# Kernel optimization log

Hardware: AMD Instinct MI355X
Metric: run time of the kernel (lower is better)

Reference implementation:

```python
import jax, jax.numpy as jnp
import numpy as np
import math

D = 32   # in_planes / d_model
T = 9    # num_contexts
L = 24   # token_len
H = 8    # nhead
HD = D // H
NEUMANN = 3
ALPHA = 0.9

def _lin(x, w, b):
    return x @ w.T + b

def _gelu(x):
    return jax.nn.gelu(x, approximate=False)

def reference(x, ln_g, ln_b, rp_w1, rp_b1, rp_w2, rp_b2, W_causal,
              mask_w, mask_b, val_w1, val_b1, val_w2, val_b2, fuse_gate,
              q_w, q_b, k_w, k_b, v_w, v_b, m_w, m_b,
              W_logit, W_ctx, rel_pos_bias, pre_prompt, conv_w, conv_b, p_w, p_b):
    b = x.shape[0]
    x_btlc = jnp.transpose(x, (0, 2, 3, 1))              # (b,t,l,c)
    # ---- rule pooling (LayerNorm -> Linear -> GELU -> Linear) ----
    pooled = x_btlc.mean(axis=(1, 2))                    # (b,c)
    mu = pooled.mean(-1, keepdims=True)
    var = pooled.var(-1, keepdims=True)
    pn = (pooled - mu) / jnp.sqrt(var + 1e-5) * ln_g + ln_b
    pooled_rule = _lin(_gelu(_lin(pn, rp_w1, rp_b1)), rp_w2, rp_b2)
    # ---- causal graph discovery ----
    A = jax.nn.softplus(W_causal) * (1.0 - jnp.eye(D, dtype=x.dtype))
    # ---- intervention engine ----
    x_obs = x_btlc.mean(axis=(1, 2))                     # (b,c)
    scale = jnp.clip(jnp.std(x_btlc, axis=(1, 2), ddof=1), 1e-3)  # torch unbiased std
    M = jax.nn.sigmoid(_lin(pooled_rule, mask_w, mask_b))
    v_raw = _lin(_gelu(_lin(pooled_rule, val_w1, val_b1)), val_w2, val_b2)
    v32 = jnp.tanh(v_raw) * scale + x_obs
    x_do = (1.0 - M) * x_obs + M * v32
    A32 = ALPHA * A / (A.sum(-1, keepdims=True) + 1e-6)  # row-normalize
    y = x_do
    for _ in range(NEUMANN):                             # fp32 Neumann series
        y = x_do + y @ A32.T
    delta = (y - x_obs)[:, None, None, :]
    fused = x_btlc + jax.nn.sigmoid(fuse_gate) * delta   # (b,t,l,c)
    # ---- cosine-sim multi-head attention with rel-pos bias & head mixing ----
    def heads(w, bb):
        h = _lin(fused, w, bb).reshape(b, T, L, H, HD).transpose(0, 1, 3, 2, 4)
        return h / jnp.linalg.norm(h, axis=-1, keepdims=True).clip(1e-12)
    q = heads(q_w, q_b); k = heads(k_w, k_b); v = heads(v_w, v_b)
    logits = jnp.einsum('bthid,bthjd->bthij', q, k) / math.sqrt(HD)
    idx = jnp.arange(L)
    rel = jnp.clip(idx[:, None] - idx[None, :] + (L - 1), 0, 2 * L - 2)
    logits = logits + rel_pos_bias[:, rel][None, None]   # (h,L,L) broadcast
    logits = jnp.einsum('bthij,hH->btHij', logits, W_logit)
    atten = jax.nn.softmax(logits, axis=-1)
    atten = jnp.einsum('bthij,hH->btHij', atten, W_ctx)
    x_att = jnp.einsum('bthij,bthjd->bthid', atten, v)
    x_att = _lin(x_att.transpose(0, 1, 3, 2, 4).reshape(b, T, L, D), m_w, m_b)
    x_att = jnp.transpose(x_att, (0, 3, 1, 2))           # (b,c,t,l)
    # ---- prediction branch (conv over contexts + linear over tokens) ----
    pre = jnp.broadcast_to(pre_prompt, (b, D, 1, L))
    con = jnp.concatenate([x_att[:, :, :T - 1], pre], axis=2)   # (b,c,T,L)
    p = jax.lax.conv_general_dilated(con, conv_w, (1, 1), 'VALID',
        dimension_numbers=('NCHW', 'OIHW', 'NCHW')) + conv_b[None, :, None, None]
    p = jax.nn.relu(p)                                   # ConvNormAct act; norm=identity at init
    p = _lin(p, p_w, p_b)                                # Linear(token_len, token_len)
    p = x_att[:, :, T - 1:] - p
    return jnp.concatenate([x_att[:, :, :T - 1], p], axis=2)


def setup_inputs() -> dict:
    key = jax.random.key(0)
    ks = jax.random.split(key, 24)
    B = 4096
    def r(i, sh, s=0.02):
        return jax.random.normal(ks[i], sh, jnp.float32) * s
    return dict(
        x=jax.random.normal(ks[0], (B, D, T, L), jnp.float32),
        ln_g=jnp.ones((D,), jnp.float32), ln_b=jnp.zeros((D,), jnp.float32),
        rp_w1=r(1, (D, D)), rp_b1=jnp.zeros((D,), jnp.float32),
        rp_w2=r(2, (D, D)), rp_b2=jnp.zeros((D,), jnp.float32),
        W_causal=r(3, (D, D)),
        mask_w=r(4, (D, D)), mask_b=jnp.zeros((D,), jnp.float32),
        val_w1=r(5, (D, D)), val_b1=jnp.zeros((D,), jnp.float32),
        val_w2=r(6, (D, D)), val_b2=jnp.zeros((D,), jnp.float32),
        fuse_gate=jnp.float32(0.5),
        q_w=r(7, (D, D)), q_b=jnp.zeros((D,), jnp.float32),
        k_w=r(8, (D, D)), k_b=jnp.zeros((D,), jnp.float32),
        v_w=r(9, (D, D)), v_b=jnp.zeros((D,), jnp.float32),
        m_w=r(10, (D, D)), m_b=jnp.zeros((D,), jnp.float32),
        W_logit=jnp.eye(H, dtype=jnp.float32) + r(11, (H, H), 0.01),
        W_ctx=jnp.eye(H, dtype=jnp.float32) + r(12, (H, H), 0.01),
        rel_pos_bias=r(13, (H, 2 * L - 1)),
        pre_prompt=r(14, (1, D, 1, L)),
        conv_w=r(15, (D, D, T, 1)), conv_b=jnp.zeros((D,), jnp.float32),
        p_w=r(16, (L, L)), p_b=jnp.zeros((L,), jnp.float32),
    )
```

## Files before the change

kernel.cpp:

```cpp
#include <hip/hip_runtime.h>
#include <hip/hip_bf16.h>

#define DD 32
#define TT 9
#define LL 24
#define HH 8
#define NPOS 216
#define RPB_W 47
#define ALPHA 0.9f

__device__ __forceinline__ float gelu_exact(float x) {
    return 0.5f * x * (1.0f + erff(x * 0.7071067811865476f));
}
__device__ __forceinline__ float sigmoidf_(float x) { return 1.0f / (1.0f + expf(-x)); }


__global__ void k0_prep(const float* __restrict__ wcausal,
                        const float* __restrict__ w_logit,
                        const float* __restrict__ rpb,
                        float* __restrict__ ws) {
    __shared__ float A[DD][DD];
    __shared__ float rs[DD];
    int tid = threadIdx.x;
    int i = tid >> 5, j = tid & 31;
    float a = (i == j) ? 0.0f : log1pf(expf(wcausal[tid]));
    A[i][j] = a;
    __syncthreads();
    if (j == 0) {
        float s = 0.0f;
        for (int k = 0; k < DD; k++) s += A[i][k];
        rs[i] = ALPHA / (s + 1e-6f);
    }
    __syncthreads();
    ws[tid] = A[i][j] * rs[i];
    if (tid < 64) ws[1024 + tid] = 0.5f * w_logit[tid];
    if (tid < 384) {
        int H = tid / 48, r = tid % 48;
        float v = 0.0f;
        if (r < RPB_W) {
            for (int h = 0; h < HH; h++) v += w_logit[h * HH + H] * rpb[h * RPB_W + r];
        }
        ws[1088 + tid] = v;
    }
}

__global__ __launch_bounds__(256) void k1a(const float* __restrict__ x,
                                           float* __restrict__ sp, float* __restrict__ sq) {
    int b = blockIdx.x, tid = threadIdx.x;
    int c = tid >> 3, r = tid & 7;
    const float4* x4 = (const float4*)(x + (size_t)b * (DD * NPOS) + (size_t)c * NPOS);
    float s = 0.0f, q = 0.0f;
    for (int k = r; k < 54; k += 8) {
        float4 v = x4[k];
        s += v.x + v.y + v.z + v.w;
        q += v.x * v.x + v.y * v.y + v.z * v.z + v.w * v.w;
    }
    for (int m = 1; m < 8; m <<= 1) { s += __shfl_xor(s, m); q += __shfl_xor(q, m); }
    if (r == 0) { sp[b * DD + c] = s; sq[b * DD + c] = q; }
}

__global__ __launch_bounds__(64) void k1b(
    const float* __restrict__ ln_g, const float* __restrict__ ln_b,
    const float* __restrict__ rp_w1, const float* __restrict__ rp_b1,
    const float* __restrict__ rp_w2, const float* __restrict__ rp_b2,
    const float* __restrict__ mask_w, const float* __restrict__ mask_b,
    const float* __restrict__ val_w1, const float* __restrict__ val_b1,
    const float* __restrict__ val_w2, const float* __restrict__ val_b2,
    const float* __restrict__ fuse_gate, const float* __restrict__ ws,
    float* __restrict__ sp , const float* __restrict__ sq)
{
    __shared__ float W[6][1024];
    __shared__ float V[7][32];
    int tid = threadIdx.x;
    for (int idx = tid; idx < 1024; idx += 64) {
        W[0][idx] = rp_w1[idx]; W[1][idx] = rp_w2[idx]; W[2][idx] = mask_w[idx];
        W[3][idx] = val_w1[idx]; W[4][idx] = val_w2[idx]; W[5][idx] = ws[idx];
    }
    if (tid < 32) {
        V[0][tid] = ln_g[tid]; V[1][tid] = ln_b[tid]; V[2][tid] = rp_b1[tid];
        V[3][tid] = rp_b2[tid]; V[4][tid] = mask_b[tid]; V[5][tid] = val_b1[tid];
        V[6][tid] = val_b2[tid];
    }
    __syncthreads();
    int b = blockIdx.x * 64 + tid;

    float pooled[32], scl[32];
    const float4* sp4 = (const float4*)(sp + (size_t)b * 32);
    const float4* sq4 = (const float4*)(sq + (size_t)b * 32);
    #pragma unroll
    for (int k = 0; k < 8; k++) {
        float4 sv = sp4[k], qv = sq4[k];
        float ss[4] = {sv.x, sv.y, sv.z, sv.w};
        float qq[4] = {qv.x, qv.y, qv.z, qv.w};
        #pragma unroll
        for (int m = 0; m < 4; m++) {
            int c = 4 * k + m;
            float p = ss[m] * (1.0f / NPOS);
            pooled[c] = p;
            float var1 = (qq[m] - (float)NPOS * p * p) * (1.0f / (NPOS - 1));
            scl[c] = fmaxf(sqrtf(fmaxf(var1, 0.0f)), 1e-3f);
        }
    }
    float mu = 0.0f;
    #pragma unroll
    for (int c = 0; c < 32; c++) mu += pooled[c];
    mu *= (1.0f / 32.0f);
    float vv = 0.0f;
    #pragma unroll
    for (int c = 0; c < 32; c++) { float d = pooled[c] - mu; vv += d * d; }
    vv *= (1.0f / 32.0f);
    float inv = rsqrtf(vv + 1e-5f);
    float pn[32];
    #pragma unroll
    for (int c = 0; c < 32; c++) pn[c] = (pooled[c] - mu) * inv * V[0][c] + V[1][c];

    float h1[32];
    #pragma unroll
    for (int i = 0; i < 32; i++) {
        float acc = V[2][i];
        #pragma unroll
        for (int j = 0; j < 32; j++) acc += pn[j] * W[0][i * 32 + j];
        h1[i] = gelu_exact(acc);
    }
    float pr[32];
    #pragma unroll
    for (int i = 0; i < 32; i++) {
        float acc = V[3][i];
        #pragma unroll
        for (int j = 0; j < 32; j++) acc += h1[j] * W[1][i * 32 + j];
        pr[i] = acc;
    }
    float g1[32];
    #pragma unroll
    for (int i = 0; i < 32; i++) {
        float acc = V[5][i];
        #pragma unroll
        for (int j = 0; j < 32; j++) acc += pr[j] * W[3][i * 32 + j];
        g1[i] = gelu_exact(acc);
    }
    float xd[32];
    #pragma unroll
    for (int i = 0; i < 32; i++) {
        float am = V[4][i];
        #pragma unroll
        for (int j = 0; j < 32; j++) am += pr[j] * W[2][i * 32 + j];
        float M = sigmoidf_(am);
        float av = V[6][i];
        #pragma unroll
        for (int j = 0; j < 32; j++) av += g1[j] * W[4][i * 32 + j];
        float v32 = tanhf(av) * scl[i] + pooled[i];
        xd[i] = (1.0f - M) * pooled[i] + M * v32;
    }
    float y[32];
    #pragma unroll
    for (int c = 0; c < 32; c++) y[c] = xd[c];
    for (int it = 0; it < 3; it++) {
        float ny[32];
        #pragma unroll
        for (int i = 0; i < 32; i++) {
            float acc = xd[i];
            #pragma unroll
            for (int j = 0; j < 32; j++) acc += y[j] * W[5][i * 32 + j];
            ny[i] = acc;
        }
        #pragma unroll
        for (int c = 0; c < 32; c++) y[c] = ny[c];
    }
    float g = sigmoidf_(fuse_gate[0]);
    float4* dout4 = (float4*)(sp + (size_t)b * 32);
    #pragma unroll
    for (int k = 0; k < 8; k++) {
        float4 o;
        o.x = g * (y[4 * k + 0] - pooled[4 * k + 0]);
        o.y = g * (y[4 * k + 1] - pooled[4 * k + 1]);
        o.z = g * (y[4 * k + 2] - pooled[4 * k + 2]);
        o.w = g * (y[4 * k + 3] - pooled[4 * k + 3]);
        dout4[k] = o;
    }
}

__global__ __launch_bounds__(192) void k2_attn(
    const float* __restrict__ x,
    const float* __restrict__ ws,
    const float* __restrict__ delta,
    const float* __restrict__ q_w, const float* __restrict__ q_b,
    const float* __restrict__ k_w, const float* __restrict__ k_b,
    const float* __restrict__ v_w, const float* __restrict__ v_b,
    const float* __restrict__ m_w, const float* __restrict__ m_b,
    const float* __restrict__ w_ctx,
    float* __restrict__ out)
{
    __shared__ float r1[3456];
    __shared__ float r2[5824];
    __shared__ float msc[640];
    float* fusedf = r1;
    float* qsf = r1 + 864;
    float* ksf = r1 + 1728;
    float* vsf = r1 + 2592;
    float* wqf = r2;
    float* wkf = r2 + 1024;
    float* wvf = r2 + 2048;
    float* lg2 = r2;
    float* wmf = r2 + 4800;
    float* bqf = msc, *bkf = msc + 32, *bvf = msc + 64, *bmf = msc + 96;
    float* wl05f = msc + 128;
    float* wcf = msc + 192;
    float* rpmf = msc + 256;

    int blk = blockIdx.x;
    int b = blk / TT, t = blk % TT;
    int tid = threadIdx.x;

    for (int idx = tid; idx < 768; idx += 192) {
        int m = idx >> 8, r = idx & 255;
        int i = r >> 3, jq = r & 7;
        const float* src = (m == 0) ? q_w : (m == 1) ? k_w : v_w;
        float* dst = (m == 0) ? wqf : (m == 1) ? wkf : wvf;
        float4 v = ((const float4*)src)[r];
        int col = i ^ (4 * jq);
        dst[(4 * jq + 0) * 32 + col] = v.x;
        dst[(4 * jq + 1) * 32 + col] = v.y;
        dst[(4 * jq + 2) * 32 + col] = v.z;
        dst[(4 * jq + 3) * 32 + col] = v.w;
    }
    if (tid < 32) { bqf[tid] = q_b[tid]; bkf[tid] = k_b[tid]; bvf[tid] = v_b[tid]; bmf[tid] = m_b[tid]; }
    else if (tid < 96) wl05f[tid - 32] = ws[1024 + tid - 32];
    else if (tid < 160) wcf[tid - 96] = w_ctx[tid - 96];
    for (int idx = tid; idx < 384; idx += 192) rpmf[idx] = ws[1088 + idx];
    {
        int c = tid / 6, k = tid % 6;
        const float4* p = (const float4*)(x + (size_t)b * (DD * NPOS) + (size_t)c * NPOS + t * LL);
        float4 v = p[k];
        float gd = delta[b * DD + c];
        int l0 = 4 * k;
        fusedf[(l0 + 0) * 36 + c] = v.x + gd;
        fusedf[(l0 + 1) * 36 + c] = v.y + gd;
        fusedf[(l0 + 2) * 36 + c] = v.z + gd;
        fusedf[(l0 + 3) * 36 + c] = v.w + gd;
    }
    __syncthreads();

    {
        int l = tid >> 3, q = tid & 7;
        float4 aq = *(const float4*)&bqf[4 * q];
        float4 ak = *(const float4*)&bkf[4 * q];
        float4 av = *(const float4*)&bvf[4 * q];
        #pragma unroll
        for (int jq = 0; jq < 8; jq++) {
            float4 f4 = *(const float4*)&fusedf[l * 36 + 4 * jq];
            float fv[4] = {f4.x, f4.y, f4.z, f4.w};
            #pragma unroll
            for (int jj = 0; jj < 4; jj++) {
                int j = 4 * jq + jj;
                int sw = (4 * q) ^ (j & 28);
                float f = fv[jj];
                float4 w0 = *(const float4*)&wqf[j * 32 + sw];
                float4 w1 = *(const float4*)&wkf[j * 32 + sw];
                float4 w2 = *(const float4*)&wvf[j * 32 + sw];
                aq.x += f * w0.x; aq.y += f * w0.y; aq.z += f * w0.z; aq.w += f * w0.w;
                ak.x += f * w1.x; ak.y += f * w1.y; ak.z += f * w1.z; ak.w += f * w1.w;
                av.x += f * w2.x; av.y += f * w2.y; av.z += f * w2.z; av.w += f * w2.w;
            }
        }
        float nq = 1.0f / fmaxf(sqrtf(aq.x*aq.x + aq.y*aq.y + aq.z*aq.z + aq.w*aq.w), 1e-12f);
        float nk = 1.0f / fmaxf(sqrtf(ak.x*ak.x + ak.y*ak.y + ak.z*ak.z + ak.w*ak.w), 1e-12f);
        float nv = 1.0f / fmaxf(sqrtf(av.x*av.x + av.y*av.y + av.z*av.z + av.w*av.w), 1e-12f);
        aq.x *= nq; aq.y *= nq; aq.z *= nq; aq.w *= nq;
        ak.x *= nk; ak.y *= nk; ak.z *= nk; ak.w *= nk;
        av.x *= nv; av.y *= nv; av.z *= nv; av.w *= nv;
        *(float4*)&qsf[l * 36 + 4 * q] = aq;
        *(float4*)&ksf[l * 36 + 4 * q] = ak;
        *(float4*)&vsf[l * 36 + 4 * q] = av;
    }
    __syncthreads();

    for (int idx = tid; idx < 256; idx += 192) {
        int i = idx >> 3, jq = idx & 7;
        float4 v = ((const float4*)m_w)[idx];
        int col = i ^ (4 * jq);
        wmf[(4 * jq + 0) * 32 + col] = v.x;
        wmf[(4 * jq + 1) * 32 + col] = v.y;
        wmf[(4 * jq + 2) * 32 + col] = v.z;
        wmf[(4 * jq + 3) * 32 + col] = v.w;
    }
    {
        int h = tid & 7, i2 = tid >> 3;
        float4 q4 = *(const float4*)&qsf[i2 * 36 + 4 * h];
        float row[24];
        #pragma unroll
        for (int j = 0; j < 24; j++) {
            float4 k4 = *(const float4*)&ksf[j * 36 + 4 * h];
            row[j] = q4.x * k4.x + q4.y * k4.y + q4.z * k4.z + q4.w * k4.w;
        }
        #pragma unroll
        for (int j = 0; j < 24; j++) lg2[i2 * 196 + j * 8 + h] = row[j];
    }
    __syncthreads();

    float sm[24];
    {
        {
            int H = tid & 7, i = tid >> 3;
            float wlc[8];
            #pragma unroll
            for (int h = 0; h < 8; h++) wlc[h] = wl05f[h * 8 + H];
            float mx = -1e30f;
            #pragma unroll
            for (int j = 0; j < 24; j++) {
                float4 ta = *(const float4*)&lg2[i * 196 + j * 8];
                float4 tb = *(const float4*)&lg2[i * 196 + j * 8 + 4];
                float a = rpmf[H * 48 + (i - j + 23)];
                a += ta.x * wlc[0] + ta.y * wlc[1] + ta.z * wlc[2] + ta.w * wlc[3]
                   + tb.x * wlc[4] + tb.y * wlc[5] + tb.z * wlc[6] + tb.w * wlc[7];
                sm[j] = a;
                mx = fmaxf(mx, a);
            }
            float s = 0.0f;
            #pragma unroll
            for (int j = 0; j < 24; j++) { float e = __expf(sm[j] - mx); sm[j] = e; s += e; }
            float inv = 1.0f / s;
            #pragma unroll
            for (int j = 0; j < 24; j++) sm[j] *= inv;
        }
        __syncthreads();
        {
            int H = tid & 7, i = tid >> 3;
            #pragma unroll
            for (int j = 0; j < 24; j++) lg2[i * 196 + j * 8 + H] = sm[j];
        }
    }
    __syncthreads();

    {
        int l = tid >> 3, q = tid & 7;
        float wcc[8];
        #pragma unroll
        for (int h = 0; h < 8; h++) wcc[h] = wcf[h * 8 + q];
        float4 acc = {0.0f, 0.0f, 0.0f, 0.0f};
        #pragma unroll
        for (int j = 0; j < 24; j++) {
            float4 ta = *(const float4*)&lg2[l * 196 + j * 8];
            float4 tb = *(const float4*)&lg2[l * 196 + j * 8 + 4];
            float a = ta.x * wcc[0] + ta.y * wcc[1] + ta.z * wcc[2] + ta.w * wcc[3]
                    + tb.x * wcc[4] + tb.y * wcc[5] + tb.z * wcc[6] + tb.w * wcc[7];
            float4 v4 = *(const float4*)&vsf[j * 36 + 4 * q];
            acc.x += a * v4.x; acc.y += a * v4.y; acc.z += a * v4.z; acc.w += a * v4.w;
        }
        *(float4*)&fusedf[l * 36 + 4 * q] = acc;
    }
    __syncthreads();

    {
        int l = tid >> 3, q = tid & 7;
        float4 acc = *(const float4*)&bmf[4 * q];
        #pragma unroll
        for (int cq = 0; cq < 8; cq++) {
            float4 f4 = *(const float4*)&fusedf[l * 36 + 4 * cq];
            float fv[4] = {f4.x, f4.y, f4.z, f4.w};
            #pragma unroll
            for (int cc = 0; cc < 4; cc++) {
                int c = 4 * cq + cc;
                int sw = (4 * q) ^ (c & 28);
                float f = fv[cc];
                float4 w4 = *(const float4*)&wmf[c * 32 + sw];
                acc.x += f * w4.x; acc.y += f * w4.y; acc.z += f * w4.z; acc.w += f * w4.w;
            }
        }
        float* resf = qsf;
        resf[(4 * q + 0) * 25 + l] = acc.x;
        resf[(4 * q + 1) * 25 + l] = acc.y;
        resf[(4 * q + 2) * 25 + l] = acc.z;
        resf[(4 * q + 3) * 25 + l] = acc.w;
    }
    __syncthreads();

    {
        const float* resf = qsf;
        int c = tid / 6, k = tid - c * 6;
        float4 v;
        v.x = resf[c * 25 + 4 * k + 0];
        v.y = resf[c * 25 + 4 * k + 1];
        v.z = resf[c * 25 + 4 * k + 2];
        v.w = resf[c * 25 + 4 * k + 3];
        float4* o4 = (float4*)(out + (size_t)b * (DD * NPOS) + (size_t)c * NPOS + t * LL);
        o4[k] = v;
    }
}

__global__ __launch_bounds__(192) void k3_pred(
    const float* __restrict__ pre_prompt,
    const float* __restrict__ conv_w, const float* __restrict__ conv_b,
    const float* __restrict__ p_w, const float* __restrict__ p_b,
    float* __restrict__ out)
{
    __shared__ float conf[DD * NPOS];
    __shared__ __hip_bfloat16 cwh[DD * 324];
    __shared__ float pbuff[DD * 25];
    __shared__ __hip_bfloat16 pwh[24 * 28];
    __shared__ float pbv[24], cbv[32];
    int b = blockIdx.x, tid = threadIdx.x;

    const float4* o4 = (const float4*)(out + (size_t)b * (DD * NPOS));
    for (int idx = tid; idx < 1728; idx += 192) {
        int flat = idx * 4;
        int t = (flat % NPOS) / LL;
        float4 v;
        if (t < 8) {
            v = o4[idx];
        } else {
            int c = flat / NPOS, l = flat % LL;
            v = ((const float4*)pre_prompt)[(c * LL + l) >> 2];
        }
        *(float4*)&conf[flat] = v;
    }
    for (int idx = tid; idx < 2304; idx += 192) {
        float4 v = ((const float4*)conv_w)[idx];
        int flat = idx * 4;
        float vv[4] = {v.x, v.y, v.z, v.w};
        #pragma unroll
        for (int e = 0; e < 4; e++) {
            int f = flat + e;
            int co = f / 288, r = f - co * 288;
            int ci = r / 9, ttt = r - ci * 9;
            cwh[co * 324 + ci * 10 + ttt] = __float2bfloat16(vv[e]);
        }
    }
    for (int idx = tid; idx < 144; idx += 192) {
        float4 v = ((const float4*)p_w)[idx];
        int flat = idx * 4;
        float vv[4] = {v.x, v.y, v.z, v.w};
        #pragma unroll
        for (int e = 0; e < 4; e++) {
            int f = flat + e;
            int row = f / 24, col = f - row * 24;
            pwh[row * 28 + col] = __float2bfloat16(vv[e]);
        }
    }
    if (tid < 24) pbv[tid] = p_b[tid];
    if (tid >= 32 && tid < 64) cbv[tid - 32] = conv_b[tid - 32];
    __syncthreads();

    {
        int co = tid / 6, ql = tid - co * 6;
        float cb = cbv[co];
        float4 acc = {cb, cb, cb, cb};
        const float4* cf4 = (const float4*)conf;
        for (int ci = 0; ci < 32; ci++) {
            const uint32_t* wp = (const uint32_t*)&cwh[co * 324 + ci * 10];
            #pragma unroll
            for (int p = 0; p < 4; p++) {
                uint32_t u = wp[p];
                float w0 = __uint_as_float(u << 16);
                float w1 = __uint_as_float(u & 0xffff0000u);
                float4 v0 = cf4[ci * 54 + (2 * p) * 6 + ql];
                float4 v1 = cf4[ci * 54 + (2 * p + 1) * 6 + ql];
                acc.x += w0 * v0.x + w1 * v1.x;
                acc.y += w0 * v0.y + w1 * v1.y;
                acc.z += w0 * v0.z + w1 * v1.z;
                acc.w += w0 * v0.w + w1 * v1.w;
            }
            float w8 = __bfloat162float(cwh[co * 324 + ci * 10 + 8]);
            float4 v8 = cf4[ci * 54 + 48 + ql];
            acc.x += w8 * v8.x; acc.y += w8 * v8.y; acc.z += w8 * v8.z; acc.w += w8 * v8.w;
        }
        pbuff[co * 25 + 4 * ql + 0] = fmaxf(acc.x, 0.0f);
        pbuff[co * 25 + 4 * ql + 1] = fmaxf(acc.y, 0.0f);
        pbuff[co * 25 + 4 * ql + 2] = fmaxf(acc.z, 0.0f);
        pbuff[co * 25 + 4 * ql + 3] = fmaxf(acc.w, 0.0f);
    }
    __syncthreads();

    {
        int c = tid / 6, ql = tid - c * 6;
        float accv[4] = {pbv[4 * ql + 0], pbv[4 * ql + 1], pbv[4 * ql + 2], pbv[4 * ql + 3]};
        #pragma unroll
        for (int lp = 0; lp < 24; lp += 2) {
            float pv0 = pbuff[c * 25 + lp];
            float pv1 = pbuff[c * 25 + lp + 1];
            #pragma unroll
            for (int e = 0; e < 4; e++) {
                uint32_t u = *(const uint32_t*)&pwh[(4 * ql + e) * 28 + lp];
                accv[e] += pv0 * __uint_as_float(u << 16) + pv1 * __uint_as_float(u & 0xffff0000u);
            }
        }
        float4* op = (float4*)(out + (size_t)b * (DD * NPOS) + (size_t)c * NPOS + 8 * LL);
        float4 xa = op[ql];
        float4 r;
        r.x = xa.x - accv[0]; r.y = xa.y - accv[1]; r.z = xa.z - accv[2]; r.w = xa.w - accv[3];
        op[ql] = r;
    }
}

extern "C" void kernel_launch(void* const* d_in, const int* in_sizes, int n_in,
                              void* d_out, int out_size, void* d_ws, size_t ws_size,
                              hipStream_t stream) {
    const float* x        = (const float*)d_in[0];
    const float* ln_g     = (const float*)d_in[1];
    const float* ln_b     = (const float*)d_in[2];
    const float* rp_w1    = (const float*)d_in[3];
    const float* rp_b1    = (const float*)d_in[4];
    const float* rp_w2    = (const float*)d_in[5];
    const float* rp_b2    = (const float*)d_in[6];
    const float* W_causal = (const float*)d_in[7];
    const float* mask_w   = (const float*)d_in[8];
    const float* mask_b   = (const float*)d_in[9];
    const float* val_w1   = (const float*)d_in[10];
    const float* val_b1   = (const float*)d_in[11];
    const float* val_w2   = (const float*)d_in[12];
    const float* val_b2   = (const float*)d_in[13];
    const float* fuse_g   = (const float*)d_in[14];
    const float* q_w      = (const float*)d_in[15];
    const float* q_b      = (const float*)d_in[16];
    const float* k_w      = (const float*)d_in[17];
    const float* k_b      = (const float*)d_in[18];
    const float* v_w      = (const float*)d_in[19];
    const float* v_b      = (const float*)d_in[20];
    const float* m_w      = (const float*)d_in[21];
    const float* m_b      = (const float*)d_in[22];
    const float* W_logit  = (const float*)d_in[23];
    const float* W_ctx    = (const float*)d_in[24];
    const float* rel_pb   = (const float*)d_in[25];
    const float* pre_pr   = (const float*)d_in[26];
    const float* conv_w   = (const float*)d_in[27];
    const float* conv_b   = (const float*)d_in[28];
    const float* p_w      = (const float*)d_in[29];
    const float* p_b      = (const float*)d_in[30];
    float* out = (float*)d_out;

    int B = in_sizes[0] / (DD * NPOS);

    float* ws = (float*)d_ws;
    float* sp = ws + 2048;
    float* sq = sp + (size_t)B * 32;

    hipLaunchKernelGGL(k0_prep, dim3(1), dim3(1024), 0, stream, W_causal, W_logit, rel_pb, ws);
    hipLaunchKernelGGL(k1a, dim3(B), dim3(256), 0, stream, x, sp, sq);
    hipLaunchKernelGGL(k1b, dim3(B / 64), dim3(64), 0, stream,
                       ln_g, ln_b, rp_w1, rp_b1, rp_w2, rp_b2,
                       mask_w, mask_b, val_w1, val_b1, val_w2, val_b2,
                       fuse_g, ws, sp, sq);
    hipLaunchKernelGGL(k2_attn, dim3(B * TT), dim3(192), 0, stream,
                       x, ws, sp, q_w, q_b, k_w, k_b, v_w, v_b, m_w, m_b,
                       W_ctx, out);
    hipLaunchKernelGGL(k3_pred, dim3(B), dim3(192), 0, stream,
                       pre_pr, conv_w, conv_b, p_w, p_b, out);
}
```

Baseline: 1.153 ms.

## Register-block attention stages over three rows and widen prediction kernel block

The QKV projection now gives each 64-thread wave one matrix (Q, K or V), and each thread computes three token rows, so every weight float4 read from LDS is reused three times. The QK logits, the context mixing and the output projection are likewise blocked over three rows but run on only the first wave of 64 threads, which cuts LDS weight traffic at the cost of idling two of the three waves in those stages. Separately, k3_pred is launched with 256 threads, so its staging loops into shared memory run with more threads while the compute stages stay limited to 192. This trades parallelism for reuse and may lengthen the serial stages in k2_attn.

```diff
diff --git a/kernel.cpp b/kernel.cpp
--- a/kernel.cpp
+++ b/kernel.cpp
@@ -241,36 +241,40 @@
     __syncthreads();
 
     {
-        int l = tid >> 3, q = tid & 7;
-        float4 aq = *(const float4*)&bqf[4 * q];
-        float4 ak = *(const float4*)&bkf[4 * q];
-        float4 av = *(const float4*)&bvf[4 * q];
+        int m = tid >> 6;
+        int g = (tid >> 3) & 7, q = tid & 7;
+        const float* wmat = (m == 0) ? wqf : (m == 1) ? wkf : wvf;
+        const float* bias = (m == 0) ? bqf : (m == 1) ? bkf : bvf;
+        float* dst       = (m == 0) ? qsf : (m == 1) ? ksf : vsf;
+        float4 bq = *(const float4*)&bias[4 * q];
+        float4 a0 = bq, a1 = bq, a2 = bq;
         #pragma unroll
         for (int jq = 0; jq < 8; jq++) {
-            float4 f4 = *(const float4*)&fusedf[l * 36 + 4 * jq];
-            float fv[4] = {f4.x, f4.y, f4.z, f4.w};
+            float4 f0 = *(const float4*)&fusedf[(g + 0) * 36 + 4 * jq];
+            float4 f1 = *(const float4*)&fusedf[(g + 8) * 36 + 4 * jq];
+            float4 f2 = *(const float4*)&fusedf[(g + 16) * 36 + 4 * jq];
+            float f0v[4] = {f0.x, f0.y, f0.z, f0.w};
+            float f1v[4] = {f1.x, f1.y, f1.z, f1.w};
+            float f2v[4] = {f2.x, f2.y, f2.z, f2.w};
             #pragma unroll
             for (int jj = 0; jj < 4; jj++) {
                 int j = 4 * jq + jj;
                 int sw = (4 * q) ^ (j & 28);
-                float f = fv[jj];
-                float4 w0 = *(const float4*)&wqf[j * 32 + sw];
-                float4 w1 = *(const float4*)&wkf[j * 32 + sw];
-                float4 w2 = *(const float4*)&wvf[j * 32 + sw];
-                aq.x += f * w0.x; aq.y += f * w0.y; aq.z += f * w0.z; aq.w += f * w0.w;
-                ak.x += f * w1.x; ak.y += f * w1.y; ak.z += f * w1.z; ak.w += f * w1.w;
-                av.x += f * w2.x; av.y += f * w2.y; av.z += f * w2.z; av.w += f * w2.w;
+                float4 w = *(const float4*)&wmat[j * 32 + sw];
+                a0.x += f0v[jj] * w.x; a0.y += f0v[jj] * w.y; a0.z += f0v[jj] * w.z; a0.w += f0v[jj] * w.w;
+                a1.x += f1v[jj] * w.x; a1.y += f1v[jj] * w.y; a1.z += f1v[jj] * w.z; a1.w += f1v[jj] * w.w;
+                a2.x += f2v[jj] * w.x; a2.y += f2v[jj] * w.y; a2.z += f2v[jj] * w.z; a2.w += f2v[jj] * w.w;
             }
         }
-        float nq = 1.0f / fmaxf(sqrtf(aq.x*aq.x + aq.y*aq.y + aq.z*aq.z + aq.w*aq.w), 1e-12f);
-        float nk = 1.0f / fmaxf(sqrtf(ak.x*ak.x + ak.y*ak.y + ak.z*ak.z + ak.w*ak.w), 1e-12f);
-        float nv = 1.0f / fmaxf(sqrtf(av.x*av.x + av.y*av.y + av.z*av.z + av.w*av.w), 1e-12f);
-        aq.x *= nq; aq.y *= nq; aq.z *= nq; aq.w *= nq;
-        ak.x *= nk; ak.y *= nk; ak.z *= nk; ak.w *= nk;
-        av.x *= nv; av.y *= nv; av.z *= nv; av.w *= nv;
-        *(float4*)&qsf[l * 36 + 4 * q] = aq;
-        *(float4*)&ksf[l * 36 + 4 * q] = ak;
-        *(float4*)&vsf[l * 36 + 4 * q] = av;
+        float n0 = 1.0f / fmaxf(sqrtf(a0.x*a0.x + a0.y*a0.y + a0.z*a0.z + a0.w*a0.w), 1e-12f);
+        float n1 = 1.0f / fmaxf(sqrtf(a1.x*a1.x + a1.y*a1.y + a1.z*a1.z + a1.w*a1.w), 1e-12f);
+        float n2 = 1.0f / fmaxf(sqrtf(a2.x*a2.x + a2.y*a2.y + a2.z*a2.z + a2.w*a2.w), 1e-12f);
+        a0.x *= n0; a0.y *= n0; a0.z *= n0; a0.w *= n0;
+        a1.x *= n1; a1.y *= n1; a1.z *= n1; a1.w *= n1;
+        a2.x *= n2; a2.y *= n2; a2.z *= n2; a2.w *= n2;
+        *(float4*)&dst[(g + 0) * 36 + 4 * q] = a0;
+        *(float4*)&dst[(g + 8) * 36 + 4 * q] = a1;
+        *(float4*)&dst[(g + 16) * 36 + 4 * q] = a2;
     }
     __syncthreads();
 
@@ -283,17 +287,18 @@
         wmf[(4 * jq + 2) * 32 + col] = v.z;
         wmf[(4 * jq + 3) * 32 + col] = v.w;
     }
-    {
-        int h = tid & 7, i2 = tid >> 3;
-        float4 q4 = *(const float4*)&qsf[i2 * 36 + 4 * h];
-        float row[24];
+    if (tid < 64) {
+        int h = tid & 7, g = tid >> 3;
+        float4 q0 = *(const float4*)&qsf[(g + 0) * 36 + 4 * h];
+        float4 q1 = *(const float4*)&qsf[(g + 8) * 36 + 4 * h];
+        float4 q2 = *(const float4*)&qsf[(g + 16) * 36 + 4 * h];
         #pragma unroll
         for (int j = 0; j < 24; j++) {
             float4 k4 = *(const float4*)&ksf[j * 36 + 4 * h];
-            row[j] = q4.x * k4.x + q4.y * k4.y + q4.z * k4.z + q4.w * k4.w;
-        }
-        #pragma unroll
-        for (int j = 0; j < 24; j++) lg2[i2 * 196 + j * 8 + h] = row[j];
+            lg2[(g + 0) * 196 + j * 8 + h] = q0.x * k4.x + q0.y * k4.y + q0.z * k4.z + q0.w * k4.w;
+            lg2[(g + 8) * 196 + j * 8 + h] = q1.x * k4.x + q1.y * k4.y + q1.z * k4.z + q1.w * k4.w;
+            lg2[(g + 16) * 196 + j * 8 + h] = q2.x * k4.x + q2.y * k4.y + q2.z * k4.z + q2.w * k4.w;
+        }
     }
     __syncthreads();
 
@@ -331,46 +336,69 @@
     }
     __syncthreads();
 
-    {
-        int l = tid >> 3, q = tid & 7;
+    if (tid < 64) {
+        int g = tid >> 3, q = tid & 7;
         float wcc[8];
         #pragma unroll
         for (int h = 0; h < 8; h++) wcc[h] = wcf[h * 8 + q];
-        float4 acc = {0.0f, 0.0f, 0.0f, 0.0f};
+        float4 a0 = {0,0,0,0}, a1 = {0,0,0,0}, a2 = {0,0,0,0};
         #pragma unroll
         for (int j = 0; j < 24; j++) {
-            float4 ta = *(const float4*)&lg2[l * 196 + j * 8];
-            float4 tb = *(const float4*)&lg2[l * 196 + j * 8 + 4];
-            float a = ta.x * wcc[0] + ta.y * wcc[1] + ta.z * wcc[2] + ta.w * wcc[3]
-                    + tb.x * wcc[4] + tb.y * wcc[5] + tb.z * wcc[6] + tb.w * wcc[7];
             float4 v4 = *(const float4*)&vsf[j * 36 + 4 * q];
-            acc.x += a * v4.x; acc.y += a * v4.y; acc.z += a * v4.z; acc.w += a * v4.w;
-        }
-        *(float4*)&fusedf[l * 36 + 4 * q] = acc;
-    }
-    __syncthreads();
-
-    {
-        int l = tid >> 3, q = tid & 7;
-        float4 acc = *(const float4*)&bmf[4 * q];
+            float4 ta0 = *(const float4*)&lg2[(g + 0) * 196 + j * 8];
+            float4 tb0 = *(const float4*)&lg2[(g + 0) * 196 + j * 8 + 4];
+            float4 ta1 = *(const float4*)&lg2[(g + 8) * 196 + j * 8];
+            float4 tb1 = *(const float4*)&lg2[(g + 8) * 196 + j * 8 + 4];
+            float4 ta2 = *(const float4*)&lg2[(g + 16) * 196 + j * 8];
+            float4 tb2 = *(const float4*)&lg2[(g + 16) * 196 + j * 8 + 4];
+            float m0 = ta0.x*wcc[0] + ta0.y*wcc[1] + ta0.z*wcc[2] + ta0.w*wcc[3]
+                     + tb0.x*wcc[4] + tb0.y*wcc[5] + tb0.z*wcc[6] + tb0.w*wcc[7];
+            float m1 = ta1.x*wcc[0] + ta1.y*wcc[1] + ta1.z*wcc[2] + ta1.w*wcc[3]
+                     + tb1.x*wcc[4] + tb1.y*wcc[5] + tb1.z*wcc[6] + tb1.w*wcc[7];
+            float m2 = ta2.x*wcc[0] + ta2.y*wcc[1] + ta2.z*wcc[2] + ta2.w*wcc[3]
+                     + tb2.x*wcc[4] + tb2.y*wcc[5] + tb2.z*wcc[6] + tb2.w*wcc[7];
+            a0.x += m0 * v4.x; a0.y += m0 * v4.y; a0.z += m0 * v4.z; a0.w += m0 * v4.w;
+            a1.x += m1 * v4.x; a1.y += m1 * v4.y; a1.z += m1 * v4.z; a1.w += m1 * v4.w;
+            a2.x += m2 * v4.x; a2.y += m2 * v4.y; a2.z += m2 * v4.z; a2.w += m2 * v4.w;
+        }
+        *(float4*)&fusedf[(g + 0) * 36 + 4 * q] = a0;
+        *(float4*)&fusedf[(g + 8) * 36 + 4 * q] = a1;
+        *(float4*)&fusedf[(g + 16) * 36 + 4 * q] = a2;
+    }
+    __syncthreads();
+
+    if (tid < 64) {
+        int g = tid >> 3, q = tid & 7;
+        float4 bq = *(const float4*)&bmf[4 * q];
+        float4 a0 = bq, a1 = bq, a2 = bq;
         #pragma unroll
         for (int cq = 0; cq < 8; cq++) {
-            float4 f4 = *(const float4*)&fusedf[l * 36 + 4 * cq];
-            float fv[4] = {f4.x, f4.y, f4.z, f4.w};
+            float4 f0 = *(const float4*)&fusedf[(g + 0) * 36 + 4 * cq];
+            float4 f1 = *(const float4*)&fusedf[(g + 8) * 36 + 4 * cq];
+            float4 f2 = *(const float4*)&fusedf[(g + 16) * 36 + 4 * cq];
+            float f0v[4] = {f0.x, f0.y, f0.z, f0.w};
+            float f1v[4] = {f1.x, f1.y, f1.z, f1.w};
+            float f2v[4] = {f2.x, f2.y, f2.z, f2.w};
             #pragma unroll
             for (int cc = 0; cc < 4; cc++) {
                 int c = 4 * cq + cc;
                 int sw = (4 * q) ^ (c & 28);
-                float f = fv[cc];
                 float4 w4 = *(const float4*)&wmf[c * 32 + sw];
-                acc.x += f * w4.x; acc.y += f * w4.y; acc.z += f * w4.z; acc.w += f * w4.w;
+                a0.x += f0v[cc] * w4.x; a0.y += f0v[cc] * w4.y; a0.z += f0v[cc] * w4.z; a0.w += f0v[cc] * w4.w;
+                a1.x += f1v[cc] * w4.x; a1.y += f1v[cc] * w4.y; a1.z += f1v[cc] * w4.z; a1.w += f1v[cc] * w4.w;
+                a2.x += f2v[cc] * w4.x; a2.y += f2v[cc] * w4.y; a2.z += f2v[cc] * w4.z; a2.w += f2v[cc] * w4.w;
             }
         }
         float* resf = qsf;
-        resf[(4 * q + 0) * 25 + l] = acc.x;
-        resf[(4 * q + 1) * 25 + l] = acc.y;
-        resf[(4 * q + 2) * 25 + l] = acc.z;
-        resf[(4 * q + 3) * 25 + l] = acc.w;
+        float av0[4] = {a0.x, a0.y, a0.z, a0.w};
+        float av1[4] = {a1.x, a1.y, a1.z, a1.w};
+        float av2[4] = {a2.x, a2.y, a2.z, a2.w};
+        #pragma unroll
+        for (int e = 0; e < 4; e++) {
+            resf[(4 * q + e) * 25 + (g + 0)]  = av0[e];
+            resf[(4 * q + e) * 25 + (g + 8)]  = av1[e];
+            resf[(4 * q + e) * 25 + (g + 16)] = av2[e];
+        }
     }
     __syncthreads();
 
@@ -387,7 +415,7 @@
     }
 }
 
-__global__ __launch_bounds__(192) void k3_pred(
+__global__ __launch_bounds__(256) void k3_pred(
     const float* __restrict__ pre_prompt,
     const float* __restrict__ conv_w, const float* __restrict__ conv_b,
     const float* __restrict__ p_w, const float* __restrict__ p_b,
@@ -401,7 +429,7 @@
     int b = blockIdx.x, tid = threadIdx.x;
 
     const float4* o4 = (const float4*)(out + (size_t)b * (DD * NPOS));
-    for (int idx = tid; idx < 1728; idx += 192) {
+    for (int idx = tid; idx < 1728; idx += 256) {
         int flat = idx * 4;
         int t = (flat % NPOS) / LL;
         float4 v;
@@ -413,7 +441,7 @@
         }
         *(float4*)&conf[flat] = v;
     }
-    for (int idx = tid; idx < 2304; idx += 192) {
+    for (int idx = tid; idx < 2304; idx += 256) {
         float4 v = ((const float4*)conv_w)[idx];
         int flat = idx * 4;
         float vv[4] = {v.x, v.y, v.z, v.w};
@@ -425,7 +453,7 @@
             cwh[co * 324 + ci * 10 + ttt] = __float2bfloat16(vv[e]);
         }
     }
-    for (int idx = tid; idx < 144; idx += 192) {
+    for (int idx = tid; idx < 144; idx += 256) {
         float4 v = ((const float4*)p_w)[idx];
         int flat = idx * 4;
         float vv[4] = {v.x, v.y, v.z, v.w};
@@ -440,7 +468,7 @@
     if (tid >= 32 && tid < 64) cbv[tid - 32] = conv_b[tid - 32];
     __syncthreads();
 
-    {
+    if (tid < 192) {
         int co = tid / 6, ql = tid - co * 6;
         float cb = cbv[co];
         float4 acc = {cb, cb, cb, cb};
@@ -470,7 +498,7 @@
     }
     __syncthreads();
 
-    {
+    if (tid < 192) {
         int c = tid / 6, ql = tid - c * 6;
         float accv[4] = {pbv[4 * ql + 0], pbv[4 * ql + 1], pbv[4 * ql + 2], pbv[4 * ql + 3]};
         #pragma unroll
@@ -542,6 +570,6 @@
     hipLaunchKernelGGL(k2_attn, dim3(B * TT), dim3(192), 0, stream,
                        x, ws, sp, q_w, q_b, k_w, k_b, v_w, v_b, m_w, m_b,
                        W_ctx, out);
-    hipLaunchKernelGGL(k3_pred, dim3(B), dim3(192), 0, stream,
+    hipLaunchKernelGGL(k3_pred, dim3(B), dim3(256), 0, stream,
                        pre_pr, conv_w, conv_b, p_w, p_b, out);
 }
```

Measured after the change: 1.981 ms. +71.8%, slower.
